# Kernel optimization log

Hardware: AMD Instinct MI355X
Metric: run time of the kernel (lower is better)

The kernel has to match this reference:

```python
import jax, jax.numpy as jnp
import numpy as np

B, C, K = 256, 512, 5  # k_size=5 from g_channels=512, gamma=2, b=1

def _conv1d(x, w):
    # x: (B, 1, C), w: (1, 1, K), 'same' padding, no bias
    pad = (K - 1) // 2
    return jax.lax.conv_general_dilated(
        x, w, window_strides=(1,), padding=[(pad, pad)],
        dimension_numbers=("NCH", "OIH", "NCH"))

def setup_inputs() -> dict:
    key = jax.random.key(0)
    kq, kk, kv, kwq, kwk, kwv = jax.random.split(key, 6)
    return {
        "q": jax.random.normal(kq, (B, 1, C), dtype=jnp.float32),
        "k": jax.random.normal(kk, (B, 1, C), dtype=jnp.float32),
        "v": jax.random.normal(kv, (B, 1, C), dtype=jnp.float32),
        "wq": jax.random.normal(kwq, (1, 1, K), dtype=jnp.float32) * 0.3,
        "wk": jax.random.normal(kwk, (1, 1, K), dtype=jnp.float32) * 0.3,
        "wv": jax.random.normal(kwv, (1, 1, K), dtype=jnp.float32) * 0.3,
    }

def reference(q, k, v, wq, wk, wv):
    # conv then transpose(-1,-2): (B,1,C) -> (B,C,1)
    qh = jnp.transpose(_conv1d(q, wq), (0, 2, 1))  # (B, C, 1)
    kh = jnp.transpose(_conv1d(k, wk), (0, 2, 1))  # (B, C, 1)
    vh = jnp.transpose(_conv1d(v, wv), (0, 2, 1))  # (B, C, 1)
    scale = jnp.sqrt(jnp.float32(qh.shape[-1]))    # sqrt(1) = 1, kept for fidelity
    scores = jnp.einsum("bci,bdi->bcd", qh, kh) / scale  # (B, C, C)
    attn = jax.nn.softmax(scores, axis=-1)
    weighted = jnp.einsum("bcd,bdi->bci", attn, vh)      # (B, C, 1)
    return weighted[..., None, None]  # (B, C, 1, 1, 1)
```

## Files before the change

kernel.cpp:

```cpp
#include <hip/hip_runtime.h>

constexpr int BATCH = 256;
constexpr int CH    = 512;
constexpr int KS    = 5;
constexpr int PAD   = (KS - 1) / 2;

__global__ __launch_bounds__(CH, 2) void attn1d_kernel(
    const float* __restrict__ q, const float* __restrict__ k, const float* __restrict__ v,
    const float* __restrict__ wq, const float* __restrict__ wk, const float* __restrict__ wv,
    float* __restrict__ out)
{
    __shared__ float sq[CH], sk[CH], sv[CH];
    __shared__ float kh[CH], vh[CH];
    __shared__ float wred_max[8], wred_min[8];
    __shared__ float s_kmax, s_kmin;

    const int b = blockIdx.x;
    const int t = threadIdx.x;

    sq[t] = q[b * CH + t];
    sk[t] = k[b * CH + t];
    sv[t] = v[b * CH + t];

    float w_q[KS], w_k[KS], w_v[KS];
#pragma unroll
    for (int j = 0; j < KS; ++j) { w_q[j] = wq[j]; w_k[j] = wk[j]; w_v[j] = wv[j]; }
    __syncthreads();

    float aq = 0.f, ak = 0.f, av = 0.f;
#pragma unroll
    for (int j = 0; j < KS; ++j) {
        const int idx = t + j - PAD;
        if (idx >= 0 && idx < CH) {
            aq = fmaf(sq[idx], w_q[j], aq);
            ak = fmaf(sk[idx], w_k[j], ak);
            av = fmaf(sv[idx], w_v[j], av);
        }
    }
    kh[t] = ak;
    vh[t] = av;

    float lmax = ak, lmin = ak;
#pragma unroll
    for (int off = 32; off > 0; off >>= 1) {
        lmax = fmaxf(lmax, __shfl_down(lmax, off, 64));
        lmin = fminf(lmin, __shfl_down(lmin, off, 64));
    }
    const int wave = t >> 6;
    if ((t & 63) == 0) { wred_max[wave] = lmax; wred_min[wave] = lmin; }
    __syncthreads();
    if (t == 0) {
        float m = wred_max[0], n = wred_min[0];
#pragma unroll
        for (int i = 1; i < 8; ++i) { m = fmaxf(m, wred_max[i]); n = fminf(n, wred_min[i]); }
        s_kmax = m; s_kmin = n;
    }
    __syncthreads();

    const float qc = aq;
    const float m = (qc >= 0.f) ? qc * s_kmax : qc * s_kmin;

    float den = 0.f, num = 0.f;
    const float4* kh4 = (const float4*)kh;
    const float4* vh4 = (const float4*)vh;
#pragma unroll 4
    for (int d4 = 0; d4 < CH / 4; ++d4) {
        const float4 kk = kh4[d4];
        const float4 vv = vh4[d4];
        const float e0 = __expf(fmaf(qc, kk.x, -m));
        const float e1 = __expf(fmaf(qc, kk.y, -m));
        const float e2 = __expf(fmaf(qc, kk.z, -m));
        const float e3 = __expf(fmaf(qc, kk.w, -m));
        den += (e0 + e1) + (e2 + e3);
        num = fmaf(e0, vv.x, num);
        num = fmaf(e1, vv.y, num);
        num = fmaf(e2, vv.z, num);
        num = fmaf(e3, vv.w, num);
    }

    out[b * CH + t] = num / den;
}

extern "C" void kernel_launch(void* const* d_in, const int* in_sizes, int n_in,
                              void* d_out, int out_size, void* d_ws, size_t ws_size,
                              hipStream_t stream) {
    const float* q  = (const float*)d_in[0];
    const float* k  = (const float*)d_in[1];
    const float* v  = (const float*)d_in[2];
    const float* wq = (const float*)d_in[3];
    const float* wk = (const float*)d_in[4];
    const float* wv = (const float*)d_in[5];
    float* out = (float*)d_out;

    attn1d_kernel<<<BATCH, CH, 0, stream>>>(q, k, v, wq, wk, wv, out);
}
```

Before: 75.53 us.

## Split conv and attention into two kernels, pre-scale q by log2e, use exp2f

Moves the convolution and the per-batch k max/min reduction into a separate kernel that writes qh, kh, vh and the extrema to workspace. A second kernel then computes the softmax-weighted sum, reading k and v from global memory (through cache) instead of LDS. q is pre-multiplied by log2(e) so exp2f can replace __expf, the max subtraction uses fmaxf instead of a branch, and the unroll factor goes up. The split adds a second launch and a round trip through global memory, in exchange for dropping the LDS reads in the inner loop and the block-wide sync.

Result: slower. 85.72 us (+13.5%).

```diff
diff --git a/kernel.cpp b/kernel.cpp
--- a/kernel.cpp
+++ b/kernel.cpp
@@ -5,15 +5,16 @@
 constexpr int KS    = 5;
 constexpr int PAD   = (KS - 1) / 2;
 
-__global__ __launch_bounds__(CH, 2) void attn1d_kernel(
+#define LOG2E 1.4426950408889634f
+
+__global__ __launch_bounds__(CH, 2) void conv_kernel(
     const float* __restrict__ q, const float* __restrict__ k, const float* __restrict__ v,
     const float* __restrict__ wq, const float* __restrict__ wk, const float* __restrict__ wv,
-    float* __restrict__ out)
+    float* __restrict__ qh, float* __restrict__ kh, float* __restrict__ vh,
+    float* __restrict__ kmax, float* __restrict__ kmin)
 {
     __shared__ float sq[CH], sk[CH], sv[CH];
-    __shared__ float kh[CH], vh[CH];
     __shared__ float wred_max[8], wred_min[8];
-    __shared__ float s_kmax, s_kmin;
 
     const int b = blockIdx.x;
     const int t = threadIdx.x;
@@ -37,8 +38,9 @@
             av = fmaf(sv[idx], w_v[j], av);
         }
     }
-    kh[t] = ak;
-    vh[t] = av;
+    qh[b * CH + t] = aq * LOG2E;
+    kh[b * CH + t] = ak;
+    vh[b * CH + t] = av;
 
     float lmax = ak, lmin = ak;
 #pragma unroll
@@ -53,24 +55,36 @@
         float m = wred_max[0], n = wred_min[0];
 #pragma unroll
         for (int i = 1; i < 8; ++i) { m = fmaxf(m, wred_max[i]); n = fminf(n, wred_min[i]); }
-        s_kmax = m; s_kmin = n;
+        kmax[b] = m;
+        kmin[b] = n;
     }
-    __syncthreads();
+}
 
-    const float qc = aq;
-    const float m = (qc >= 0.f) ? qc * s_kmax : qc * s_kmin;
+__global__ __launch_bounds__(CH, 2) void attn_kernel(
+    const float* __restrict__ qh, const float* __restrict__ kh, const float* __restrict__ vh,
+    const float* __restrict__ kmax, const float* __restrict__ kmin,
+    float* __restrict__ out)
+{
+    const int b = blockIdx.x;
+    const int t = threadIdx.x;
+
+    const float qc = qh[b * CH + t];
+    const float kmx = kmax[b];
+    const float kmn = kmin[b];
+    const float m2 = fmaxf(qc * kmx, qc * kmn);
+
+    const float4* __restrict__ kh4 = (const float4*)(kh + b * CH);
+    const float4* __restrict__ vh4 = (const float4*)(vh + b * CH);
 
     float den = 0.f, num = 0.f;
-    const float4* kh4 = (const float4*)kh;
-    const float4* vh4 = (const float4*)vh;
-#pragma unroll 4
+#pragma unroll 8
     for (int d4 = 0; d4 < CH / 4; ++d4) {
         const float4 kk = kh4[d4];
         const float4 vv = vh4[d4];
-        const float e0 = __expf(fmaf(qc, kk.x, -m));
-        const float e1 = __expf(fmaf(qc, kk.y, -m));
-        const float e2 = __expf(fmaf(qc, kk.z, -m));
-        const float e3 = __expf(fmaf(qc, kk.w, -m));
+        const float e0 = exp2f(fmaf(qc, kk.x, -m2));
+        const float e1 = exp2f(fmaf(qc, kk.y, -m2));
+        const float e2 = exp2f(fmaf(qc, kk.z, -m2));
+        const float e3 = exp2f(fmaf(qc, kk.w, -m2));
         den += (e0 + e1) + (e2 + e3);
         num = fmaf(e0, vv.x, num);
         num = fmaf(e1, vv.y, num);
@@ -92,5 +106,13 @@
     const float* wv = (const float*)d_in[5];
     float* out = (float*)d_out;
 
-    attn1d_kernel<<<BATCH, CH, 0, stream>>>(q, k, v, wq, wk, wv, out);
+    float* ws   = (float*)d_ws;
+    float* qh   = ws;
+    float* kh   = ws + BATCH * CH;
+    float* vh   = ws + 2 * BATCH * CH;
+    float* kmax = ws + 3 * BATCH * CH;
+    float* kmin = kmax + BATCH;
+
+    conv_kernel<<<BATCH, CH, 0, stream>>>(q, k, v, wq, wk, wv, qh, kh, vh, kmax, kmin);
+    attn_kernel<<<BATCH, CH, 0, stream>>>(qh, kh, vh, kmax, kmin, out);
 }
```
